# Kernel optimization log

Measured on AMD Instinct MI355X. Metric: run time of the kernel, lower is better.

Reference implementation:

```python
import jax, jax.numpy as jnp
import numpy as np

B, T, C, H = 4, 2048, 1024, 16
HD = C // H  # head dim = 64


def setup_inputs() -> dict:
    key = jax.random.key(0)
    ks = jax.random.split(key, 9)
    s = 1.0 / np.sqrt(C)
    return {
        "x": jax.random.normal(ks[0], (B, T, C), dtype=jnp.float32),
        "Wq": jax.random.normal(ks[1], (C, C), dtype=jnp.float32) * s,
        "bq": jnp.zeros((C,), dtype=jnp.float32),
        "Wk": jax.random.normal(ks[2], (C, C), dtype=jnp.float32) * s,
        "bk": jnp.zeros((C,), dtype=jnp.float32),
        "Wv": jax.random.normal(ks[3], (C, C), dtype=jnp.float32) * s,
        "bv": jnp.zeros((C,), dtype=jnp.float32),
        "Wo": jax.random.normal(ks[4], (C, C), dtype=jnp.float32) * s,
        "bo": jnp.zeros((C,), dtype=jnp.float32),
    }


def reference(x, Wq, bq, Wk, bk, Wv, bv, Wo, bo):
    # Linear projections (torch Linear: x @ W.T + b)
    q = x @ Wq.T + bq
    k = x @ Wk.T + bk
    v = x @ Wv.T + bv
    # [B, T, C] -> [B, H, T, HD]
    def split(t):
        return t.reshape(B, T, H, HD).transpose(0, 2, 1, 3)
    q, k, v = split(q), split(k), split(v)
    scores = jnp.einsum("bhqd,bhkd->bhqk", q, k) / np.sqrt(HD).astype(np.float32)
    causal = jnp.tril(jnp.ones((T, T), dtype=bool))
    scores = jnp.where(causal[None, None], scores, -jnp.inf)
    attn = jax.nn.softmax(scores, axis=-1)
    # dropout layers are identity in eval mode
    out = jnp.einsum("bhqk,bhkd->bhqd", attn, v)
    out = out.transpose(0, 2, 1, 3).reshape(B, T, C)
    return out @ Wo.T + bo
```

## Files before the change

### kernel.cpp

```cpp
#include <hip/hip_runtime.h>
#include <hip/hip_bf16.h>

#define DEVI __device__ __forceinline__

typedef __attribute__((ext_vector_type(4))) float f32x4;
typedef __attribute__((ext_vector_type(16))) float f32x16;
typedef __attribute__((ext_vector_type(8))) short bf16x8;
typedef __attribute__((ext_vector_type(4))) short bf16x4;
typedef __attribute__((ext_vector_type(4))) int i32x4;

constexpr int Bb = 4, Tt = 2048, Cc = 1024, Hh = 16, HDd = 64;
constexpr int Mm = Bb * Tt;

DEVI short f2bf(float f) {
    union { float f; unsigned u; } x; x.f = f;
    unsigned r = x.u + 0x7FFFu + ((x.u >> 16) & 1u);
    return (short)(r >> 16);
}

DEVI int cvtpk(float lo, float hi) {
    int r;
    asm("v_cvt_pk_bf16_f32 %0, %1, %2" : "=v"(r) : "v"(lo), "v"(hi));
    return r;
}

DEVI float fexp2(float x) { return __builtin_amdgcn_exp2f(x); }

DEVI void gload_lds16(const void* g, void* l) {
    __builtin_amdgcn_global_load_lds(
        (const __attribute__((address_space(1))) unsigned int*)g,
        (__attribute__((address_space(3))) unsigned int*)l, 16, 0, 0);
}

__global__ void cvt_kernel(const float* __restrict__ s, short* __restrict__ d, int n8) {
    int i = blockIdx.x * 256 + threadIdx.x;
    if (i < n8) {
        const float4* sp = (const float4*)s;
        float4 a = sp[2 * i], b = sp[2 * i + 1];
        short tmp[8];
        tmp[0] = f2bf(a.x); tmp[1] = f2bf(a.y); tmp[2] = f2bf(a.z); tmp[3] = f2bf(a.w);
        tmp[4] = f2bf(b.x); tmp[5] = f2bf(b.y); tmp[6] = f2bf(b.z); tmp[7] = f2bf(b.w);
        *(bf16x8*)(d + 8 * (size_t)i) = *(bf16x8*)tmp;
    }
}

__global__ void cvtw_kernel(const float* __restrict__ w0, const float* __restrict__ w1,
                            const float* __restrict__ w2, const float* __restrict__ w3,
                            short* __restrict__ d0, short* __restrict__ d1,
                            short* __restrict__ d2, short* __restrict__ d3) {
    const int sel = blockIdx.y;
    const float* s = sel == 0 ? w0 : sel == 1 ? w1 : sel == 2 ? w2 : w3;
    short* d = sel == 0 ? d0 : sel == 1 ? d1 : sel == 2 ? d2 : d3;
    const int i = blockIdx.x * 256 + threadIdx.x;
    const float4* sp = (const float4*)s;
    float4 a = sp[2 * i], b = sp[2 * i + 1];
    short tmp[8];
    tmp[0] = f2bf(a.x); tmp[1] = f2bf(a.y); tmp[2] = f2bf(a.z); tmp[3] = f2bf(a.w);
    tmp[4] = f2bf(b.x); tmp[5] = f2bf(b.y); tmp[6] = f2bf(b.z); tmp[7] = f2bf(b.w);
    *(bf16x8*)(d + 8 * (size_t)i) = *(bf16x8*)tmp;
}

struct GemmAcc { f32x4 acc[4][4]; };

DEVI void gemm_core(const short* __restrict__ A, const short* __restrict__ Bw,
                    int Kdim, int bm, int bn, int tid,
                    short (*As)[64], short (*Bs)[64], GemmAcc& G)
{
    const int lane = tid & 63, wid = tid >> 6;
    const int wr = wid >> 1, wc = wid & 1;
    const int lrow = lane >> 3;
    const int lcol = (lane & 7) * 8;

    for (int k0 = 0; k0 < Kdim; k0 += 64) {
        #pragma unroll
        for (int c = 0; c < 4; ++c) {
            const int chunk = wid * 4 + c;
            const int row = chunk * 8 + lrow;
            gload_lds16(A  + (size_t)(bm + row) * Kdim + k0 + lcol, &As[chunk * 8][0]);
            gload_lds16(Bw + (size_t)(bn + row) * Kdim + k0 + lcol, &Bs[chunk * 8][0]);
        }
        __syncthreads();
        const int rr = lane & 15;
        #pragma unroll
        for (int kk = 0; kk < 64; kk += 32) {
            const int koff = kk + (lane >> 4) * 8;
            bf16x8 af[4], bfr[4];
            #pragma unroll
            for (int m_ = 0; m_ < 4; ++m_)
                af[m_] = *(const bf16x8*)&As[wr * 64 + m_ * 16 + rr][koff];
            #pragma unroll
            for (int n_ = 0; n_ < 4; ++n_)
                bfr[n_] = *(const bf16x8*)&Bs[wc * 64 + n_ * 16 + rr][koff];
            #pragma unroll
            for (int m_ = 0; m_ < 4; ++m_)
                #pragma unroll
                for (int n_ = 0; n_ < 4; ++n_)
                    G.acc[m_][n_] = __builtin_amdgcn_mfma_f32_16x16x32_bf16(
                        af[m_], bfr[n_], G.acc[m_][n_], 0, 0, 0);
        }
        __syncthreads();
    }
}

__global__ __launch_bounds__(256, 2)
void gemm_qkv(const short* __restrict__ A,
              const short* __restrict__ Wq, const short* __restrict__ Wk,
              const short* __restrict__ Wv,
              const float* __restrict__ bq, const float* __restrict__ bk,
              const float* __restrict__ bv,
              short* __restrict__ Qo, short* __restrict__ Ko, short* __restrict__ Vto,
              float sq)
{
    __shared__ __align__(16) short As[128][64];
    __shared__ __align__(16) short Bs[128][64];
    const int sec = blockIdx.y >> 3;
    const int bn = (blockIdx.y & 7) * 128;
    const int bm = blockIdx.x * 128;
    const short* Bw = sec == 0 ? Wq : sec == 1 ? Wk : Wv;
    const float* bias = sec == 0 ? bq : sec == 1 ? bk : bv;
    const float scale = sec == 0 ? sq : 1.0f;

    GemmAcc G = {};
    gemm_core(A, Bw, Cc, bm, bn, threadIdx.x, As, Bs, G);

    const int lane = threadIdx.x & 63, wid = threadIdx.x >> 6;
    const int wr = wid >> 1, wc = wid & 1;
    const int cidx = lane & 15;
    const int r4 = (lane >> 4) * 4;
    #pragma unroll
    for (int n_ = 0; n_ < 4; ++n_) {
        const int col = bn + wc * 64 + n_ * 16 + cidx;
        const float bv_ = bias[col];
        #pragma unroll
        for (int m_ = 0; m_ < 4; ++m_) {
            const int rowb = bm + wr * 64 + m_ * 16 + r4;
            if (sec == 2) {
                const int h_ = col >> 6, d_ = col & 63;
                const int b_ = rowb >> 11, t_ = rowb & 2047;
                short tmp[4];
                #pragma unroll
                for (int i = 0; i < 4; ++i) tmp[i] = f2bf((G.acc[m_][n_][i] + bv_));
                *(bf16x4*)(Vto + ((size_t)((b_ * Hh + h_) * HDd + d_)) * Tt + t_) = *(bf16x4*)tmp;
            } else {
                short* C = sec == 0 ? Qo : Ko;
                #pragma unroll
                for (int i = 0; i < 4; ++i)
                    C[(size_t)(rowb + i) * Cc + col] = f2bf((G.acc[m_][n_][i] + bv_) * scale);
            }
        }
    }
}

__global__ __launch_bounds__(256, 2)
void gemm_out(const short* __restrict__ A, const short* __restrict__ Bw,
              const float* __restrict__ bias, float* __restrict__ Cout)
{
    __shared__ __align__(16) short As[128][64];
    __shared__ __align__(16) short Bs[128][64];
    const int bm = blockIdx.x * 128;
    const int bn = blockIdx.y * 128;
    GemmAcc G = {};
    gemm_core(A, Bw, Cc, bm, bn, threadIdx.x, As, Bs, G);

    const int lane = threadIdx.x & 63, wid = threadIdx.x >> 6;
    const int wr = wid >> 1, wc = wid & 1;
    const int cidx = lane & 15;
    const int r4 = (lane >> 4) * 4;
    #pragma unroll
    for (int n_ = 0; n_ < 4; ++n_) {
        const int col = bn + wc * 64 + n_ * 16 + cidx;
        const float bv_ = bias[col];
        #pragma unroll
        for (int m_ = 0; m_ < 4; ++m_) {
            const int rowb = bm + wr * 64 + m_ * 16 + r4;
            #pragma unroll
            for (int i = 0; i < 4; ++i)
                Cout[(size_t)(rowb + i) * Cc + col] = G.acc[m_][n_][i] + bv_;
        }
    }
}

template<bool DIAG>
DEVI void attn_tile(int kv0, const short (*Kt)[64], const short (*Vd)[64],
                    const bf16x8 (&qf)[4], int lane, int qrow,
                    f32x16 (&oacc)[2], float &mrow, float &lsum)
{
    const int q31 = lane & 31;
    const int hi  = lane >> 5;

    f32x16 sacc[2] = {};
    __builtin_amdgcn_s_setprio(1);
    #pragma unroll
    for (int ks = 0; ks < 4; ++ks) {
        #pragma unroll
        for (int nb = 0; nb < 2; ++nb) {
            const int row = nb * 32 + q31;
            bf16x8 kf = *(const bf16x8*)&Kt[row][(((ks << 1) | hi) ^ (row & 7)) * 8];
            sacc[nb] = __builtin_amdgcn_mfma_f32_32x32x16_bf16(kf, qf[ks], sacc[nb], 0, 0, 0);
        }
    }
    __builtin_amdgcn_s_setprio(0);

    if (DIAG) {
        #pragma unroll
        for (int nb = 0; nb < 2; ++nb)
            #pragma unroll
            for (int r = 0; r < 16; ++r) {
                const int kv = kv0 + nb * 32 + (r & 3) + 8 * (r >> 2) + 4 * hi;
                if (kv > qrow) sacc[nb][r] = -1e30f;
            }
    }

    float tm[16];
    #pragma unroll
    for (int r = 0; r < 16; ++r) tm[r] = fmaxf(sacc[0][r], sacc[1][r]);
    #pragma unroll
    for (int st = 8; st >= 1; st >>= 1)
        #pragma unroll
        for (int r = 0; r < st; ++r) tm[r] = fmaxf(tm[r], tm[r + st]);
    const float pmax = fmaxf(tm[0], __shfl_xor(tm[0], 32, 64));

    if (!__all(pmax <= mrow + 8.0f)) {
        const float mnew = fmaxf(mrow, pmax);
        const float alpha = fexp2(mrow - mnew);
        mrow = mnew;
        lsum *= alpha;
        #pragma unroll
        for (int r = 0; r < 16; ++r) {
            const float ar = __shfl(alpha, (r & 3) + 8 * (r >> 2) + 4 * hi, 32);
            oacc[0][r] *= ar;
            oacc[1][r] *= ar;
        }
    }

    #pragma unroll
    for (int nb = 0; nb < 2; ++nb)
        #pragma unroll
        for (int r = 0; r < 16; ++r)
            sacc[nb][r] = fexp2(sacc[nb][r] - mrow);
    float ps[16];
    #pragma unroll
    for (int r = 0; r < 16; ++r) ps[r] = sacc[0][r] + sacc[1][r];
    #pragma unroll
    for (int st = 8; st >= 1; st >>= 1)
        #pragma unroll
        for (int r = 0; r < st; ++r) ps[r] += ps[r + st];
    lsum += ps[0];

    #pragma unroll
    for (int ks = 0; ks < 4; ++ks) {
        const int n = ks >> 1, b8 = (ks & 1) * 8;
        int x0 = cvtpk(sacc[n][b8 + 0], sacc[n][b8 + 1]);
        int x1 = cvtpk(sacc[n][b8 + 2], sacc[n][b8 + 3]);
        int y0 = cvtpk(sacc[n][b8 + 4], sacc[n][b8 + 5]);
        int y1 = cvtpk(sacc[n][b8 + 6], sacc[n][b8 + 7]);
        asm volatile("v_permlane32_swap_b32 %0, %1" : "+v"(x0), "+v"(y0));
        asm volatile("v_permlane32_swap_b32 %0, %1" : "+v"(x1), "+v"(y1));
        i32x4 w; w.x = x0; w.y = x1; w.z = y0; w.w = y1;
        const bf16x8 pav = __builtin_bit_cast(bf16x8, w);
        __builtin_amdgcn_s_setprio(1);
        #pragma unroll
        for (int nb = 0; nb < 2; ++nb) {
            const int row = nb * 32 + q31;
            bf16x8 vf = *(const bf16x8*)&Vd[row][(((ks << 1) | hi) ^ (row & 7)) * 8];
            oacc[nb] = __builtin_amdgcn_mfma_f32_32x32x16_bf16(pav, vf, oacc[nb], 0, 0, 0);
        }
        __builtin_amdgcn_s_setprio(0);
    }
}

DEVI void attn_run(int qt, const short* __restrict__ Q, short* __restrict__ O,
                   const short* kbase, const short* vbase, size_t baseRow, int h,
                   int lane, int wid, short (*Kb)[64][64], short (*Vb)[64][64])
{
    const int q0 = qt * 128;
    const int q31 = lane & 31;
    const int hi = lane >> 5;
    const int qrow = q0 + wid * 32 + q31;

    const short* qptr = Q + (baseRow + qrow) * Cc + h * HDd + hi * 8;
    bf16x8 qf[4];
    #pragma unroll
    for (int ks = 0; ks < 4; ++ks) qf[ks] = *(const bf16x8*)(qptr + ks * 16);

    f32x16 oacc[2] = {};
    float mrow = -1e30f, lsum = 0.f;
    const int NT = 2 * qt + 2;

    auto STAGE = [&](int bsel, int kv0) {
        #pragma unroll
        for (int j = 0; j < 2; ++j) {
            const int r0 = wid * 16 + j * 8;
            const int row = r0 + (lane >> 3);
            const int sc = ((lane & 7) ^ (row & 7)) * 8;
            gload_lds16(kbase + (size_t)(kv0 + row) * Cc + sc, &Kb[bsel][r0][0]);
            gload_lds16(vbase + (size_t)row * Tt + kv0 + sc, &Vb[bsel][r0][0]);
        }
    };

    STAGE(0, 0);
    int buf = 0;
    for (int kt = 0; kt < NT; ++kt) {
        if (kt + 1 < NT) {
            STAGE(buf ^ 1, (kt + 1) * 64);
            asm volatile("s_waitcnt vmcnt(4)" ::: "memory");
        } else {
            asm volatile("s_waitcnt vmcnt(0)" ::: "memory");
        }
        __builtin_amdgcn_s_barrier();
        __builtin_amdgcn_sched_barrier(0);
        if (kt >= NT - 2)
            attn_tile<true >(kt * 64, Kb[buf], Vb[buf], qf, lane, qrow, oacc, mrow, lsum);
        else
            attn_tile<false>(kt * 64, Kb[buf], Vb[buf], qf, lane, qrow, oacc, mrow, lsum);
        __builtin_amdgcn_s_barrier();
        buf ^= 1;
    }

    lsum += __shfl_xor(lsum, 32, 64);
    #pragma unroll
    for (int r = 0; r < 16; ++r) {
        const int crow = (r & 3) + 8 * (r >> 2) + 4 * hi;
        const float ri = __builtin_amdgcn_rcpf(__shfl(lsum, crow, 32));
        const size_t rb = (baseRow + q0 + wid * 32 + crow) * Cc + h * HDd + q31;
        O[rb]      = f2bf(oacc[0][r] * ri);
        O[rb + 32] = f2bf(oacc[1][r] * ri);
    }
}

__global__ __launch_bounds__(256, 3)
void attn_kernel(const short* __restrict__ Q, const short* __restrict__ K,
                 const short* __restrict__ Vt, short* __restrict__ O)
{
    const int bid = blockIdx.x;
    const int bh = (bid & 7) + 8 * ((bid >> 3) & 7);
    const int qt = 15 - (bid >> 6);
    const int b = bh >> 4, h = bh & 15;
    const size_t baseRow = (size_t)b * Tt;
    const int tid = threadIdx.x, lane = tid & 63, wid = tid >> 6;

    __shared__ __align__(16) short Kb[2][64][64];
    __shared__ __align__(16) short Vb[2][64][64];

    const short* kbase = K + baseRow * Cc + h * HDd;
    const short* vbase = Vt + (size_t)bh * HDd * Tt;

    attn_run(qt, Q, O, kbase, vbase, baseRow, h, lane, wid, Kb, Vb);
}

extern "C" void kernel_launch(void* const* d_in, const int* in_sizes, int n_in,
                              void* d_out, int out_size, void* d_ws, size_t ws_size,
                              hipStream_t stream) {
    (void)in_sizes; (void)n_in; (void)out_size; (void)ws_size;
    const float* x  = (const float*)d_in[0];
    const float* Wq = (const float*)d_in[1];
    const float* bq = (const float*)d_in[2];
    const float* Wk = (const float*)d_in[3];
    const float* bk = (const float*)d_in[4];
    const float* Wv = (const float*)d_in[5];
    const float* bv = (const float*)d_in[6];
    const float* Wo = (const float*)d_in[7];
    const float* bo = (const float*)d_in[8];
    float* out = (float*)d_out;

    short* ws  = (short*)d_ws;
    short* xb  = ws;
    short* wqb = xb  + (size_t)Mm * Cc;
    short* wkb = wqb + (size_t)Cc * Cc;
    short* wvb = wkb + (size_t)Cc * Cc;
    short* wob = wvb + (size_t)Cc * Cc;
    short* Qb  = wob + (size_t)Cc * Cc;
    short* Kbg = Qb  + (size_t)Mm * Cc;
    short* Vtb = Kbg + (size_t)Mm * Cc;
    short* Ob  = Vtb + (size_t)Mm * Cc;

    const int nx8 = Mm * Cc / 8;
    const int nw8 = Cc * Cc / 8;
    cvt_kernel<<<(nx8 + 255) / 256, 256, 0, stream>>>(x, xb, nx8);
    cvtw_kernel<<<dim3(nw8 / 256, 4), 256, 0, stream>>>(Wq, Wk, Wv, Wo, wqb, wkb, wvb, wob);

    const float SCL = 0.125f * 1.44269504088896f;
    gemm_qkv<<<dim3(Mm / 128, 24), 256, 0, stream>>>(xb, wqb, wkb, wvb, bq, bk, bv,
                                                     Qb, Kbg, Vtb, SCL);

    attn_kernel<<<dim3(Tt / 128 * Bb * Hh), 256, 0, stream>>>(Qb, Kbg, Vtb, Ob);

    gemm_out<<<dim3(Mm / 128, Cc / 128), 256, 0, stream>>>(Ob, wob, bo, out);
}
```

Measured before the change: 166.7 us.

## Split long causal attention query tiles into two KV chunks with merge kernel

```diff
diff --git a/kernel.cpp b/kernel.cpp
--- a/kernel.cpp
+++ b/kernel.cpp
@@ -16,6 +16,10 @@
     union { float f; unsigned u; } x; x.f = f;
     unsigned r = x.u + 0x7FFFu + ((x.u >> 16) & 1u);
     return (short)(r >> 16);
+}
+
+DEVI float bf2f(short s) {
+    return __builtin_bit_cast(float, (unsigned)((unsigned short)s) << 16);
 }
 
 DEVI int cvtpk(float lo, float hi) {
@@ -269,14 +273,18 @@
     }
 }
 
-DEVI void attn_run(int qt, const short* __restrict__ Q, short* __restrict__ O,
-                   const short* kbase, const short* vbase, size_t baseRow, int h,
-                   int lane, int wid, short (*Kb)[64][64], short (*Vb)[64][64])
+DEVI void attn_range(int qt, int ktLo, int ktHi,
+                     const short* __restrict__ Q, short* __restrict__ O,
+                     short* __restrict__ OPpart, float* __restrict__ MP,
+                     float* __restrict__ LP,
+                     const short* kbase, const short* vbase, size_t baseRow, int h,
+                     int lane, int wid, short (*Kb)[64][64], short (*Vb)[64][64])
 {
     const int q0 = qt * 128;
     const int q31 = lane & 31;
     const int hi = lane >> 5;
     const int qrow = q0 + wid * 32 + q31;
+    const int NT = 2 * qt + 2;
 
     const short* qptr = Q + (baseRow + qrow) * Cc + h * HDd + hi * 8;
     bf16x8 qf[4];
@@ -285,7 +293,6 @@
 
     f32x16 oacc[2] = {};
     float mrow = -1e30f, lsum = 0.f;
-    const int NT = 2 * qt + 2;
 
     auto STAGE = [&](int bsel, int kv0) {
         #pragma unroll
@@ -298,10 +305,10 @@
         }
     };
 
-    STAGE(0, 0);
+    STAGE(0, ktLo * 64);
     int buf = 0;
-    for (int kt = 0; kt < NT; ++kt) {
-        if (kt + 1 < NT) {
+    for (int kt = ktLo; kt < ktHi; ++kt) {
+        if (kt + 1 < ktHi) {
             STAGE(buf ^ 1, (kt + 1) * 64);
             asm volatile("s_waitcnt vmcnt(4)" ::: "memory");
         } else {
@@ -318,23 +325,44 @@
     }
 
     lsum += __shfl_xor(lsum, 32, 64);
-    #pragma unroll
-    for (int r = 0; r < 16; ++r) {
-        const int crow = (r & 3) + 8 * (r >> 2) + 4 * hi;
-        const float ri = __builtin_amdgcn_rcpf(__shfl(lsum, crow, 32));
-        const size_t rb = (baseRow + q0 + wid * 32 + crow) * Cc + h * HDd + q31;
-        O[rb]      = f2bf(oacc[0][r] * ri);
-        O[rb + 32] = f2bf(oacc[1][r] * ri);
-    }
-}
+
+    if (OPpart == nullptr) {
+        #pragma unroll
+        for (int r = 0; r < 16; ++r) {
+            const int crow = (r & 3) + 8 * (r >> 2) + 4 * hi;
+            const float ri = __builtin_amdgcn_rcpf(__shfl(lsum, crow, 32));
+            const size_t rb = (baseRow + q0 + wid * 32 + crow) * Cc + h * HDd + q31;
+            O[rb]      = f2bf(oacc[0][r] * ri);
+            O[rb + 32] = f2bf(oacc[1][r] * ri);
+        }
+    } else {
+        #pragma unroll
+        for (int r = 0; r < 16; ++r) {
+            const int crow = (r & 3) + 8 * (r >> 2) + 4 * hi;
+            const int row = wid * 32 + crow;
+            OPpart[row * 64 + q31]      = f2bf(oacc[0][r]);
+            OPpart[row * 64 + 32 + q31] = f2bf(oacc[1][r]);
+        }
+        if (hi == 0) {
+            MP[wid * 32 + q31] = mrow;
+            LP[wid * 32 + q31] = lsum;
+        }
+    }
+}
+
+__device__ const signed char JQT[24] = {7,15,15,14,14,6,13,13,12,12,5,11,11,10,10,4,9,9,8,8,3,2,1,0};
+__device__ const signed char JCH[24] = {-1,0,1,0,1,-1,0,1,0,1,-1,0,1,0,1,-1,0,1,0,1,-1,-1,-1,-1};
 
 __global__ __launch_bounds__(256, 3)
 void attn_kernel(const short* __restrict__ Q, const short* __restrict__ K,
-                 const short* __restrict__ Vt, short* __restrict__ O)
+                 const short* __restrict__ Vt, short* __restrict__ O,
+                 short* __restrict__ OP, float* __restrict__ MP, float* __restrict__ LP)
 {
     const int bid = blockIdx.x;
     const int bh = (bid & 7) + 8 * ((bid >> 3) & 7);
-    const int qt = 15 - (bid >> 6);
+    const int job = bid >> 6;
+    const int qt = JQT[job];
+    const int ch = JCH[job];
     const int b = bh >> 4, h = bh & 15;
     const size_t baseRow = (size_t)b * Tt;
     const int tid = threadIdx.x, lane = tid & 63, wid = tid >> 6;
@@ -345,7 +373,54 @@
     const short* kbase = K + baseRow * Cc + h * HDd;
     const short* vbase = Vt + (size_t)bh * HDd * Tt;
 
-    attn_run(qt, Q, O, kbase, vbase, baseRow, h, lane, wid, Kb, Vb);
+    if (ch < 0) {
+        attn_range(qt, 0, 2 * qt + 2, Q, O, nullptr, nullptr, nullptr,
+                   kbase, vbase, baseRow, h, lane, wid, Kb, Vb);
+    } else {
+        const int qs = qt - 8;
+        const int pbase = (bh * 8 + qs) * 2 + ch;
+        const int ktLo = ch == 0 ? 0 : qt + 1;
+        const int ktHi = ch == 0 ? qt + 1 : 2 * qt + 2;
+        attn_range(qt, ktLo, ktHi, Q, O,
+                   OP + (size_t)pbase * 128 * 64, MP + pbase * 128, LP + pbase * 128,
+                   kbase, vbase, baseRow, h, lane, wid, Kb, Vb);
+    }
+}
+
+__global__ __launch_bounds__(256, 8)
+void attn_merge(const short* __restrict__ OP, const float* __restrict__ MP,
+                const float* __restrict__ LP, short* __restrict__ O)
+{
+    const int g = blockIdx.x;
+    const int bh = g >> 3, qs = g & 7;
+    const int qt = qs + 8;
+    const int b = bh >> 4, h = bh & 15;
+    const int tid = threadIdx.x;
+    const int q = tid >> 1;
+    const int dhalf = (tid & 1) * 32;
+
+    const size_t i0 = ((size_t)g * 2 + 0) * 128 + q;
+    const size_t i1 = ((size_t)g * 2 + 1) * 128 + q;
+    const float m0 = MP[i0], m1 = MP[i1];
+    const float l0 = LP[i0], l1 = LP[i1];
+    const float m = fmaxf(m0, m1);
+    float w0 = fexp2(m0 - m), w1 = fexp2(m1 - m);
+    const float ri = __builtin_amdgcn_rcpf(l0 * w0 + l1 * w1);
+    w0 *= ri; w1 *= ri;
+
+    const short* p0 = OP + i0 * 64 + dhalf;
+    const short* p1 = OP + i1 * 64 + dhalf;
+    short* po = O + ((size_t)b * Tt + qt * 128 + q) * Cc + h * HDd + dhalf;
+    #pragma unroll
+    for (int j = 0; j < 32; j += 8) {
+        bf16x8 a = *(const bf16x8*)(p0 + j);
+        bf16x8 c = *(const bf16x8*)(p1 + j);
+        short tmp[8];
+        #pragma unroll
+        for (int e = 0; e < 8; ++e)
+            tmp[e] = f2bf(bf2f(((short*)&a)[e]) * w0 + bf2f(((short*)&c)[e]) * w1);
+        *(bf16x8*)(po + j) = *(bf16x8*)tmp;
+    }
 }
 
 extern "C" void kernel_launch(void* const* d_in, const int* in_sizes, int n_in,
@@ -374,6 +449,10 @@
     short* Vtb = Kbg + (size_t)Mm * Cc;
     short* Ob  = Vtb + (size_t)Mm * Cc;
 
+    short* OPart = xb;
+    float* MPart = (float*)wqb;
+    float* LPart = (float*)wkb;
+
     const int nx8 = Mm * Cc / 8;
     const int nw8 = Cc * Cc / 8;
     cvt_kernel<<<(nx8 + 255) / 256, 256, 0, stream>>>(x, xb, nx8);
@@ -383,7 +462,8 @@
     gemm_qkv<<<dim3(Mm / 128, 24), 256, 0, stream>>>(xb, wqb, wkb, wvb, bq, bk, bv,
                                                      Qb, Kbg, Vtb, SCL);
 
-    attn_kernel<<<dim3(Tt / 128 * Bb * Hh), 256, 0, stream>>>(Qb, Kbg, Vtb, Ob);
+    attn_kernel<<<dim3(24 * 64), 256, 0, stream>>>(Qb, Kbg, Vtb, Ob, OPart, MPart, LPart);
+    attn_merge<<<dim3(512), 256, 0, stream>>>(OPart, MPart, LPart, Ob);
 
     gemm_out<<<dim3(Mm / 128, Cc / 128), 256, 0, stream>>>(Ob, wob, bo, out);
 }
```

After: 174.9 us. +4.9%, slower.
